# Performance work log

Measured on AMD Instinct MI355X. Metric: run time of the kernel, lower is better.

The kernel has to match this reference:

```python
import jax, jax.numpy as jnp
import numpy as np
from math import sqrt

DIM_KEY = 64
B, H, LQ, LK, D = 8, 8, 1024, 1024, 64


def setup_inputs() -> dict:
    key = jax.random.key(0)
    k1, k2, k3, k4 = jax.random.split(key, 4)
    return {
        "query": jax.random.normal(k1, (B, H, LQ, D), dtype=jnp.float32),
        "key": jax.random.normal(k2, (B, H, LK, D), dtype=jnp.float32),
        "value": jax.random.normal(k3, (B, H, LK, D), dtype=jnp.float32),
        "mask": jax.random.randint(k4, (B, H, LQ, LK), 0, 2, dtype=jnp.int32),
        "query_mask": jnp.ones((B, H, 1, LQ), dtype=jnp.float32),
    }


def reference(query, key, value, mask, query_mask):
    # scores: [B, H, LQ, LK]
    scores = jnp.einsum("bhqd,bhkd->bhqk", query / sqrt(DIM_KEY), key)
    scores = jnp.where(mask == 0, jnp.float32(-1e9), scores)
    attention = jax.nn.softmax(scores, axis=-1)
    # query_mask [B,H,1,LQ] -> transpose(2,3) -> [B,H,LQ,1], broadcasts over keys
    attention = attention * jnp.swapaxes(query_mask, 2, 3)
    # dropout is identity in eval/reference mode
    output = jnp.einsum("bhqk,bhkd->bhqd", attention, value)
    return output, attention
```

## Files before the change

### kernel.cpp

```cpp
#include <hip/hip_runtime.h>
#include <hip/hip_bf16.h>


typedef float  f32x4  __attribute__((ext_vector_type(4)));
typedef int    i32x4  __attribute__((ext_vector_type(4)));
typedef short  bf16x8 __attribute__((ext_vector_type(8)));
typedef short  s16x4  __attribute__((ext_vector_type(4)));
typedef short  s16x8  __attribute__((ext_vector_type(8)));

#define BH 64
#define LQN 1024
#define LKN 1024
#define DD 64
#define QT 8
#define SMEM_BYTES (QT * LKN * 4)
#define SADDR(row, cb) (((row) << 12) + ((cb) ^ (((row) & 7) << 4)))

static __device__ __forceinline__ short f2bf(float f) {
  unsigned u = __float_as_uint(f);
  unsigned r = (u + 0x7fffu + ((u >> 16) & 1u)) >> 16;
  return (short)r;
}

__global__ void cvt_k(const float* __restrict__ K, short* __restrict__ Kbf) {
  int i = blockIdx.x * 256 + threadIdx.x;
  f32x4 v = ((const f32x4*)K)[i];
  s16x4 o;
  o[0] = f2bf(v[0]); o[1] = f2bf(v[1]); o[2] = f2bf(v[2]); o[3] = f2bf(v[3]);
  ((s16x4*)Kbf)[i] = o;
}

__global__ void cvt_v(const float* __restrict__ V, short* __restrict__ Vt) {
  __shared__ float tile[64][65];
  int bh = blockIdx.x >> 4, kt = blockIdx.x & 15;
  int t = threadIdx.x;
  const float* src = V + ((size_t)bh * LKN + kt * 64) * DD;
  for (int j = 0; j < 4; ++j) {
    int f = t + j * 256;
    f32x4 v = *(const f32x4*)(src + f * 4);
    int r = f >> 4, c = (f & 15) * 4;
    tile[r][c] = v[0]; tile[r][c + 1] = v[1]; tile[r][c + 2] = v[2]; tile[r][c + 3] = v[3];
  }
  __syncthreads();
  int d = t >> 2, kc = (t & 3) * 16;
  short* dst = Vt + ((size_t)(bh * DD + d)) * LKN + kt * 64 + kc;
  s16x8 o0, o1;
  for (int j = 0; j < 8; ++j) {
    o0[j] = f2bf(tile[kc + j][d]);
    o1[j] = f2bf(tile[kc + 8 + j][d]);
  }
  *(s16x8*)dst = o0;
  *(s16x8*)(dst + 8) = o1;
}

__global__ __launch_bounds__(256, 5) void attn(
    const float* __restrict__ Qf, const short* __restrict__ Kbf,
    const short* __restrict__ Vt, const int* __restrict__ mask,
    const float* __restrict__ qmask, float* __restrict__ out,
    float* __restrict__ att) {
  extern __shared__ char smem[];
  int bh = blockIdx.x >> 7;
  int q0 = (blockIdx.x & 127) * QT;
  int w = threadIdx.x >> 6, l = threadIdx.x & 63;
  int lr = l & 15, lg = l >> 4;

  bf16x8 qa[2];
  {
    const float* qrow = Qf + ((size_t)(bh * LQN + q0 + (lr & 7))) * DD + lg * 8;
    for (int t = 0; t < 2; ++t) {
      f32x4 a = *(const f32x4*)(qrow + t * 32);
      f32x4 b = *(const f32x4*)(qrow + t * 32 + 4);
      bf16x8 q;
      for (int j = 0; j < 4; ++j) { q[j] = f2bf(a[j] * 0.125f); q[4 + j] = f2bf(b[j] * 0.125f); }
      qa[t] = q;
    }
  }

  i32x4 pm[2][4];
#pragma unroll
  for (int rr = 0; rr < 2; ++rr) {
    const int* mrow = mask + ((size_t)(bh * LQN + q0 + w * 2 + rr)) * LKN;
#pragma unroll
    for (int j = 0; j < 4; ++j)
      pm[rr][j] = *(const i32x4*)(mrow + 4 * (l + 64 * j));
  }

  for (int ks = w * 16; ks < w * 16 + 16; ++ks) {
    int kb = ks * 16;
    const short* krow = Kbf + ((size_t)(bh * LKN + kb + lr)) * DD + lg * 8;
    bf16x8 k0 = *(const bf16x8*)(krow);
    bf16x8 k1 = *(const bf16x8*)(krow + 32);
    f32x4 acc = {0.f, 0.f, 0.f, 0.f};
    acc = __builtin_amdgcn_mfma_f32_16x16x32_bf16(qa[0], k0, acc, 0, 0, 0);
    acc = __builtin_amdgcn_mfma_f32_16x16x32_bf16(qa[1], k1, acc, 0, 0, 0);
    if (lg < 2)
      for (int r = 0; r < 4; ++r)
        *(float*)(smem + SADDR(lg * 4 + r, (kb + lr) * 4)) = acc[r];
  }
  __syncthreads();

#pragma unroll
  for (int rr = 0; rr < 2; ++rr) {
    int row = w * 2 + rr;
    f32x4 v[4];
    float mx = -3.4e38f;
#pragma unroll
    for (int j = 0; j < 4; ++j) {
      v[j] = *(f32x4*)(smem + SADDR(row, 16 * (l + 64 * j)));
      i32x4 m4 = pm[rr][j];
      for (int c = 0; c < 4; ++c) v[j][c] = m4[c] ? v[j][c] : -1e9f;
      mx = fmaxf(mx, fmaxf(fmaxf(v[j][0], v[j][1]), fmaxf(v[j][2], v[j][3])));
    }
    for (int off = 32; off; off >>= 1) mx = fmaxf(mx, __shfl_xor(mx, off));
    float sum = 0.f;
    for (int j = 0; j < 4; ++j)
      for (int c = 0; c < 4; ++c) { v[j][c] = __expf(v[j][c] - mx); sum += v[j][c]; }
    for (int off = 32; off; off >>= 1) sum += __shfl_xor(sum, off);
    float qm = qmask[bh * LQN + q0 + row];
    float scale = qm / sum;
    float* arow = att + ((size_t)(bh * LQN + q0 + row)) * LKN;
    for (int j = 0; j < 4; ++j) {
      f32x4 o = v[j] * scale;
      *(f32x4*)(smem + SADDR(row, 16 * (l + 64 * j))) = o;
      *(f32x4*)(arow + 4 * (l + 64 * j)) = o;
    }
  }
  __syncthreads();

  f32x4 acc = {0.f, 0.f, 0.f, 0.f};
  const short* vrow = Vt + ((size_t)(bh * DD + w * 16 + lr)) * LKN;
  for (int kt = 0; kt < 32; ++kt) {
    int cb = kt * 128 + lg * 32;
    f32x4 lo = *(f32x4*)(smem + SADDR(lr & 7, cb));
    f32x4 hi = *(f32x4*)(smem + SADDR(lr & 7, cb + 16));
    bf16x8 a;
    for (int j = 0; j < 4; ++j) { a[j] = f2bf(lo[j]); a[4 + j] = f2bf(hi[j]); }
    bf16x8 b = *(const bf16x8*)(vrow + kt * 32 + lg * 8);
    acc = __builtin_amdgcn_mfma_f32_16x16x32_bf16(a, b, acc, 0, 0, 0);
  }
  if (lg < 2)
    for (int r = 0; r < 4; ++r) {
      int row = lg * 4 + r;
      out[((size_t)(bh * LQN + q0 + row)) * DD + w * 16 + lr] = acc[r];
    }
}

extern "C" void kernel_launch(void* const* d_in, const int* in_sizes, int n_in,
                              void* d_out, int out_size, void* d_ws, size_t ws_size,
                              hipStream_t stream) {
  const float* Q = (const float*)d_in[0];
  const float* K = (const float*)d_in[1];
  const float* V = (const float*)d_in[2];
  const int* mask = (const int*)d_in[3];
  const float* qmask = (const float*)d_in[4];
  float* out = (float*)d_out;
  float* att = out + (size_t)BH * LQN * DD;
  short* Kbf = (short*)d_ws;
  short* Vt = Kbf + (size_t)BH * LKN * DD;

  cvt_k<<<4096, 256, 0, stream>>>(K, Kbf);
  cvt_v<<<1024, 256, 0, stream>>>(V, Vt);
  attn<<<BH * (LQN / QT), 256, SMEM_BYTES, stream>>>(Q, Kbf, Vt, mask, qmask, out, att);
}
```

Before: 647.6 us.

## Double query tile to 16 rows with 8 waves and split-K PV reduction

Raises the query tile from 8 to 16 rows so the full 16-row MFMA output is used instead of wasting half of it, and moves to 512-thread blocks with 8 waves. Each wave handles half as many key blocks in QK^T. The PV product is split across two wave halves over the key dimension and their partial sums are combined through shared memory. This halves redundant K/V loads per query row and MFMA waste, at the cost of 64KB shared memory per block, extra barriers and possibly lower occupancy.

After: 555.8 us. 14.2% less time.

```diff
diff --git a/kernel.cpp b/kernel.cpp
--- a/kernel.cpp
+++ b/kernel.cpp
@@ -12,7 +12,7 @@
 #define LQN 1024
 #define LKN 1024
 #define DD 64
-#define QT 8
+#define QT 16
 #define SMEM_BYTES (QT * LKN * 4)
 #define SADDR(row, cb) (((row) << 12) + ((cb) ^ (((row) & 7) << 4)))
 
@@ -53,20 +53,20 @@
   *(s16x8*)(dst + 8) = o1;
 }
 
-__global__ __launch_bounds__(256, 5) void attn(
+__global__ __launch_bounds__(512, 4) void attn(
     const float* __restrict__ Qf, const short* __restrict__ Kbf,
     const short* __restrict__ Vt, const int* __restrict__ mask,
     const float* __restrict__ qmask, float* __restrict__ out,
     float* __restrict__ att) {
   extern __shared__ char smem[];
-  int bh = blockIdx.x >> 7;
-  int q0 = (blockIdx.x & 127) * QT;
+  int bh = blockIdx.x >> 6;
+  int q0 = (blockIdx.x & 63) * QT;
   int w = threadIdx.x >> 6, l = threadIdx.x & 63;
   int lr = l & 15, lg = l >> 4;
 
   bf16x8 qa[2];
   {
-    const float* qrow = Qf + ((size_t)(bh * LQN + q0 + (lr & 7))) * DD + lg * 8;
+    const float* qrow = Qf + ((size_t)(bh * LQN + q0 + lr)) * DD + lg * 8;
     for (int t = 0; t < 2; ++t) {
       f32x4 a = *(const f32x4*)(qrow + t * 32);
       f32x4 b = *(const f32x4*)(qrow + t * 32 + 4);
@@ -85,17 +85,17 @@
       pm[rr][j] = *(const i32x4*)(mrow + 4 * (l + 64 * j));
   }
 
-  for (int ks = w * 16; ks < w * 16 + 16; ++ks) {
-    int kb = ks * 16;
+#pragma unroll 4
+  for (int i = 0; i < 8; ++i) {
+    int kb = (w * 8 + i) * 16;
     const short* krow = Kbf + ((size_t)(bh * LKN + kb + lr)) * DD + lg * 8;
     bf16x8 k0 = *(const bf16x8*)(krow);
     bf16x8 k1 = *(const bf16x8*)(krow + 32);
     f32x4 acc = {0.f, 0.f, 0.f, 0.f};
     acc = __builtin_amdgcn_mfma_f32_16x16x32_bf16(qa[0], k0, acc, 0, 0, 0);
     acc = __builtin_amdgcn_mfma_f32_16x16x32_bf16(qa[1], k1, acc, 0, 0, 0);
-    if (lg < 2)
-      for (int r = 0; r < 4; ++r)
-        *(float*)(smem + SADDR(lg * 4 + r, (kb + lr) * 4)) = acc[r];
+    for (int r = 0; r < 4; ++r)
+      *(float*)(smem + SADDR(lg * 4 + r, (kb + lr) * 4)) = acc[r];
   }
   __syncthreads();
 
@@ -127,22 +127,32 @@
   }
   __syncthreads();
 
+  int h = w >> 2, ws = w & 3;
   f32x4 acc = {0.f, 0.f, 0.f, 0.f};
-  const short* vrow = Vt + ((size_t)(bh * DD + w * 16 + lr)) * LKN;
-  for (int kt = 0; kt < 32; ++kt) {
-    int cb = kt * 128 + lg * 32;
-    f32x4 lo = *(f32x4*)(smem + SADDR(lr & 7, cb));
-    f32x4 hi = *(f32x4*)(smem + SADDR(lr & 7, cb + 16));
+  const short* vrow = Vt + ((size_t)(bh * DD + ws * 16 + lr)) * LKN;
+#pragma unroll 4
+  for (int kt = 0; kt < 16; ++kt) {
+    int ktg = h * 16 + kt;
+    int cb = ktg * 128 + lg * 32;
+    f32x4 lo = *(f32x4*)(smem + SADDR(lr, cb));
+    f32x4 hi = *(f32x4*)(smem + SADDR(lr, cb + 16));
     bf16x8 a;
     for (int j = 0; j < 4; ++j) { a[j] = f2bf(lo[j]); a[4 + j] = f2bf(hi[j]); }
-    bf16x8 b = *(const bf16x8*)(vrow + kt * 32 + lg * 8);
+    bf16x8 b = *(const bf16x8*)(vrow + ktg * 32 + lg * 8);
     acc = __builtin_amdgcn_mfma_f32_16x16x32_bf16(a, b, acc, 0, 0, 0);
   }
-  if (lg < 2)
+  __syncthreads();
+  if (h == 1)
+    *(f32x4*)(smem + ((ws * 64 + l) << 4)) = acc;
+  __syncthreads();
+  if (h == 0) {
+    f32x4 other = *(f32x4*)(smem + ((ws * 64 + l) << 4));
+    acc += other;
     for (int r = 0; r < 4; ++r) {
       int row = lg * 4 + r;
-      out[((size_t)(bh * LQN + q0 + row)) * DD + w * 16 + lr] = acc[r];
+      out[((size_t)(bh * LQN + q0 + row)) * DD + ws * 16 + lr] = acc[r];
     }
+  }
 }
 
 extern "C" void kernel_launch(void* const* d_in, const int* in_sizes, int n_in,
@@ -160,5 +170,5 @@
 
   cvt_k<<<4096, 256, 0, stream>>>(K, Kbf);
   cvt_v<<<1024, 256, 0, stream>>>(V, Vt);
-  attn<<<BH * (LQN / QT), 256, SMEM_BYTES, stream>>>(Q, Kbf, Vt, mask, qmask, out, att);
+  attn<<<BH * (LQN / QT), 512, SMEM_BYTES, stream>>>(Q, Kbf, Vt, mask, qmask, out, att);
 }
```
